# Kernel tuning notes

Hardware: AMD Instinct MI355X
Metric: run time of the kernel (lower is better)

The kernel has to match this reference:

```python
import jax, jax.numpy as jnp
import numpy as np

B, T, S = 128, 512, 30      # batch, input temporal length, sensor channels
F_NUM, KS, NL = 64, 5, 4    # conv filters, kernel size, n conv layers
H, NC = 128, 18             # GRU hidden dim, n classes


def setup_inputs() -> dict:
    key = jax.random.key(0)
    ks = jax.random.split(key, 16)
    r = lambda i, shape, s=0.05: (jax.random.normal(ks[i], shape, jnp.float32) * s)
    return {
        "x": jax.random.normal(ks[0], (B, 1, T, S), jnp.float32),
        "conv0_w": r(1, (F_NUM, 1, KS, 1), 0.2),          # first Conv2d (in=1)
        "convs_w": r(2, (3, F_NUM, F_NUM, KS, 1), 0.05),  # conv layers 1..3
        "conv_b": r(3, (NL, F_NUM)),
        "bn_gamma": jnp.ones((NL, F_NUM), jnp.float32),
        "bn_beta": jnp.zeros((NL, F_NUM), jnp.float32),
        "bn_mean": jnp.zeros((NL, F_NUM), jnp.float32),
        "bn_var": jnp.ones((NL, F_NUM), jnp.float32),
        "wq": r(4, (F_NUM, F_NUM), 0.1),
        "wk": r(5, (F_NUM, F_NUM), 0.1),
        "wv": r(6, (F_NUM, F_NUM), 0.1),
        "sa_gamma": jnp.array([0.1], jnp.float32),
        "fc1_w": r(7, (H, S * F_NUM), 0.02),
        "fc1_b": r(8, (H,)),
        "gru_wih": r(9, (2, 3 * H, H), 0.05),
        "gru_whh": r(10, (2, 3 * H, H), 0.05),
        "gru_bih": r(11, (2, 3 * H)),
        "gru_bhh": r(12, (2, 3 * H)),
        "pred_w": r(13, (NC, H), 0.05),
        "pred_b": r(14, (NC,)),
    }


def reference(x, conv0_w, convs_w, conv_b, bn_gamma, bn_beta, bn_mean, bn_var,
              wq, wk, wv, sa_gamma, fc1_w, fc1_b,
              gru_wih, gru_whh, gru_bih, gru_bhh, pred_w, pred_b):
    eps = 1e-5

    def conv_relu_bn(y, w, b, g, be, m, v):
        # Conv2d kernel (KS,1) stride (2,1), then ReLU, then BatchNorm (eval mode)
        y = jax.lax.conv_general_dilated(
            y, w, (2, 1), 'VALID',
            dimension_numbers=('NCHW', 'OIHW', 'NCHW')) + b[None, :, None, None]
        y = jax.nn.relu(y)
        inv = g / jnp.sqrt(v + eps)
        return y * inv[None, :, None, None] + (be - m * inv)[None, :, None, None]

    x = conv_relu_bn(x, conv0_w, conv_b[0], bn_gamma[0], bn_beta[0], bn_mean[0], bn_var[0])
    for i in range(3):  # fixed small layer loop
        x = conv_relu_bn(x, convs_w[i], conv_b[i + 1], bn_gamma[i + 1],
                         bn_beta[i + 1], bn_mean[i + 1], bn_var[i + 1])

    Bn, Fn, Ln, Sn = x.shape
    # Fold time into batch: per-timestep SelfAttention over (F, S) slices, vectorized
    xs = jnp.transpose(x, (0, 2, 1, 3)).reshape(Bn * Ln, Fn, Sn)  # (N, F, S)
    f = jnp.einsum('of,nfs->nos', wq, xs)   # query (1x1 conv1d, no bias)
    g = jnp.einsum('of,nfs->nos', wk, xs)   # key
    h = jnp.einsum('of,nfs->nos', wv, xs)   # value
    scores = jnp.einsum('noi,noj->nij', f, g)         # bmm(f^T, g): (N, S, S)
    beta = jax.nn.softmax(scores, axis=1)             # softmax over dim=1 (as torch)
    o = sa_gamma[0] * jnp.einsum('nfi,nij->nfj', h, beta) + xs  # (N, F, S)

    # cat over t then permute(0,3,1,2).reshape == (B, L, F*S)
    seq = o.reshape(Bn, Ln, Fn * Sn)
    seq = jax.nn.relu(seq @ fc1_w.T + fc1_b)          # (B, L, H); dropout = eval noop
    xs_t = jnp.transpose(seq, (1, 0, 2))              # (L, B, H) seq-first for GRU

    def gru_layer(xseq, wih, whh, bih, bhh):
        Hd = whh.shape[1]
        def step(hprev, xt):
            gi = xt @ wih.T + bih
            gh = hprev @ whh.T + bhh
            ir, iz, inn = jnp.split(gi, 3, axis=-1)
            hr, hz, hn = jnp.split(gh, 3, axis=-1)
            r = jax.nn.sigmoid(ir + hr)
            z = jax.nn.sigmoid(iz + hz)
            n = jnp.tanh(inn + r * hn)
            hnew = (1.0 - z) * n + z * hprev
            return hnew, hnew
        h0 = jnp.zeros((xseq.shape[1], Hd), xseq.dtype)
        _, ys = jax.lax.scan(step, h0, xseq)
        return ys

    for l in range(2):  # 2-layer GRU (inter-layer dropout = eval noop)
        xs_t = gru_layer(xs_t, gru_wih[l], gru_whh[l], gru_bih[l], gru_bhh[l])

    return xs_t[-1] @ pred_w.T + pred_b               # (B, NC)
```

## Files before the change

kernel.cpp:

```cpp
#include <hip/hip_runtime.h>
#include <math.h>

#define EPS 1e-5f

#define B_  128
#define T0_ 512
#define S_  30
#define F_  64
#define L1_ 254
#define L2_ 125
#define L3_ 61
#define L4_ 29
#define BS_ (B_*S_)
#define N_  (B_*L4_)
#define H_  128
#define NC_ 18
#define KFS 1920

typedef __attribute__((ext_vector_type(8))) short short8;
typedef __attribute__((ext_vector_type(16))) float f32x16;

__device__ __forceinline__ uint32_t f2bf(float f) {
    uint32_t u = __float_as_uint(f);
    return (u + 0x7fffu + ((u >> 16) & 1u)) >> 16;
}

typedef const __attribute__((address_space(1))) uint32_t* gas_t;
typedef __attribute__((address_space(3))) uint32_t* las_t;
__device__ __forceinline__ void glds16(const void* g, void* l) {
    __builtin_amdgcn_global_load_lds((gas_t)g, (las_t)l, 16, 0, 0);
}

#define MFMA(a,b,c) __builtin_amdgcn_mfma_f32_32x32x16_bf16(a, b, c, 0, 0, 0)

union ABu { uint4 u; short8 s; };

__global__ __launch_bounds__(256) void prepack_kernel(
    const float* __restrict__ wcs, ushort* __restrict__ aw)
{
    int i = blockIdx.x*256 + threadIdx.x;
    int l = i / 20480, r = i - l*20480;
    int j = r & 7, f = (r >> 3) & 63, g = r >> 9;
    int chalf = g & 1, ck = (g >> 1) & 3, kh = g >> 3;
    int c = ck*16 + chalf*8 + j;
    float w = wcs[l*20480 + f*320 + c*5 + kh];
    uint32_t h = f2bf(w);
    uint32_t lo = f2bf(w - __uint_as_float(h << 16));
    aw[l*40960 + r]         = (ushort)h;
    aw[l*40960 + 20480 + r] = (ushort)lo;
}

__device__ __forceinline__ void load_areg(const ushort* __restrict__ aw_l,
                                          int f0, int tcol, int chalf,
                                          ABu* AH_, ABu* AL_)
{
    #pragma unroll
    for (int idx = 0; idx < 20; idx++) {
        int r = (idx*2 + chalf)*512 + (f0 + tcol)*8;
        AH_[idx].u = *(const uint4*)(aw_l + r);
        AL_[idx].u = *(const uint4*)(aw_l + 20480 + r);
    }
}

__device__ __forceinline__ f32x16 conv_mm_reg(
    const ABu* AH_, const ABu* AL_,
    const ushort* __restrict__ Bh, const ushort* __restrict__ Bl,
    int t, int chalf)
{
    f32x16 acc;
    #pragma unroll
    for (int i = 0; i < 16; i++) acc[i] = 0.f;
    #pragma unroll
    for (int kh = 0; kh < 5; kh++) {
        int tp = 2*t + kh;
        int sw = (tp >> 3) & 7;
        const ushort* brh = Bh + tp*64;
        const ushort* brl = Bl + tp*64;
        #pragma unroll
        for (int ck = 0; ck < 4; ck++) {
            int idx = kh*4 + ck;
            int col = (((ck*2 + chalf) ^ sw) << 3);
            short8 BH = *(const short8*)(brh + col);
            short8 BL = *(const short8*)(brl + col);
            acc = MFMA(AH_[idx].s, BH, acc);
            acc = MFMA(AH_[idx].s, BL, acc);
            acc = MFMA(AL_[idx].s, BH, acc);
        }
    }
    return acc;
}

__global__ __launch_bounds__(512, 2) void conv01_mfma(
    const float* __restrict__ x,  const float* __restrict__ w0,
    const ushort* __restrict__ aw, const float* __restrict__ cb,
    const float* __restrict__ bg, const float* __restrict__ bb,
    const float* __restrict__ bm, const float* __restrict__ bv,
    char* __restrict__ y1h, char* __restrict__ y1l)
{
    __shared__ ushort Yt[2][264*64];
    __shared__ float xl[T0_];
    __shared__ float ep0[64], ep1[64], ep2[64];
    int tid = threadIdx.x;
    int lane = tid & 63, wv = tid >> 6;
    int tcol = lane & 31, chalf = lane >> 5;
    int f0 = (wv>>2)*32, t0 = (wv&3)*32, t = t0 + tcol;

    ABu AH_[20], AL_[20];
    load_areg(aw, f0, tcol, chalf, AH_, AL_);

    int cq = tid & 15, tpb = tid >> 4, c0 = cq*4;
    float w0r[20], inv0[4], add0[4], b0r[4];
    #pragma unroll
    for (int j = 0; j < 4; j++) {
        int c = c0 + j;
        #pragma unroll
        for (int u = 0; u < 5; u++) w0r[j*5+u] = w0[c*5+u];
        float iv = bg[c]*rsqrtf(bv[c]+EPS);
        inv0[j] = iv; add0[j] = bb[c]-bm[c]*iv; b0r[j] = cb[c];
    }
    if (tid < 64) {
        float iv = bg[64+tid]*rsqrtf(bv[64+tid]+EPS);
        ep0[tid] = iv; ep1[tid] = bb[64+tid]-bm[64+tid]*iv; ep2[tid] = cb[64+tid];
    }

    for (int sl = 0; sl < 5; sl++) {
        int bs = blockIdx.x*5 + sl, b = bs/S_, s = bs - b*S_;
        xl[tid] = x[(b*T0_ + tid)*S_ + s];
        __syncthreads();
        #pragma unroll
        for (int k = 0; k < 9; k++) {
            int tp = tpb + k*32;
            if (tp < 264) {
                float v4[4];
                if (tp < L1_) {
                    float2 xa = *(const float2*)&xl[2*tp];
                    float2 xb = *(const float2*)&xl[2*tp+2];
                    float2 xc = *(const float2*)&xl[2*tp+4];
                    #pragma unroll
                    for (int j = 0; j < 4; j++) {
                        float a = b0r[j] + w0r[j*5]*xa.x + w0r[j*5+1]*xa.y
                                + w0r[j*5+2]*xb.x + w0r[j*5+3]*xb.y + w0r[j*5+4]*xc.x;
                        v4[j] = fmaxf(a, 0.f)*inv0[j] + add0[j];
                    }
                } else { v4[0]=v4[1]=v4[2]=v4[3]=0.f; }
                uint32_t h0=f2bf(v4[0]), h1=f2bf(v4[1]), h2=f2bf(v4[2]), h3=f2bf(v4[3]);
                uint2 H; H.x = h0|(h1<<16); H.y = h2|(h3<<16);
                uint2 L;
                L.x = f2bf(v4[0]-__uint_as_float(h0<<16)) | (f2bf(v4[1]-__uint_as_float(h1<<16))<<16);
                L.y = f2bf(v4[2]-__uint_as_float(h2<<16)) | (f2bf(v4[3]-__uint_as_float(h3<<16))<<16);
                int pos = tp*64 + (c0 ^ (((tp>>3)&7)<<3));
                *(uint2*)&Yt[0][pos] = H;
                *(uint2*)&Yt[1][pos] = L;
            }
        }
        __syncthreads();
        f32x16 acc = conv_mm_reg(AH_, AL_, Yt[0], Yt[1], t, chalf);
        __syncthreads();
        if (t < L2_) {
            int swzo = ((t>>1) ^ (t>>3)) & 7;
            #pragma unroll
            for (int rq = 0; rq < 4; rq++) {
                int fb = f0 + 8*rq + 4*chalf;
                uint32_t h[4], l[4];
                #pragma unroll
                for (int j = 0; j < 4; j++) {
                    int r = rq*4 + j, f = fb + j;
                    float val = fmaxf(acc[r]+ep2[f], 0.f)*ep0[f] + ep1[f];
                    h[j] = f2bf(val);
                    l[j] = f2bf(val - __uint_as_float(h[j]<<16));
                }
                int pos = ((((fb>>3) ^ swzo) << 3) + (fb & 7));
                uint2 H; H.x = h[0] | (h[1]<<16); H.y = h[2] | (h[3]<<16);
                uint2 L; L.x = l[0] | (l[1]<<16); L.y = l[2] | (l[3]<<16);
                *(uint2*)&Yt[0][t*64 + pos] = H;
                *(uint2*)&Yt[1][t*64 + pos] = L;
            }
        }
        __syncthreads();
        for (int i = tid; i < 2000; i += 512) {
            int pl = i >= 1000, jj = pl ? i-1000 : i;
            int tr = jj >> 3, p = jj & 7;
            int q = p ^ ((tr>>1) & 7);
            uint4 v = *(const uint4*)&Yt[pl][tr*64 + q*8];
            *(uint4*)((pl ? y1l : y1h) + (size_t)bs*16000 + tr*128 + p*16) = v;
        }
    }
}

__global__ __launch_bounds__(512, 2) void conv2_mfma(
    const ushort* __restrict__ aw, const float* __restrict__ cb,
    const float* __restrict__ bg, const float* __restrict__ bb,
    const float* __restrict__ bm, const float* __restrict__ bv,
    char* __restrict__ yh, char* __restrict__ yl)
{
    __shared__ ushort Yt[2][2][2][132*64];
    __shared__ float ep0[64], ep1[64], ep2[64];
    int tid = threadIdx.x;
    int lane = tid & 63, wv = tid >> 6;
    int tcol = lane & 31, chalf = lane >> 5;
    int slw = wv >> 2, f0 = ((wv>>1)&1)*32, t0 = (wv&1)*32, t = t0 + tcol;
    int blk = blockIdx.x;

    ABu AH_[20], AL_[20];
    load_areg(aw + 40960, f0, tcol, chalf, AH_, AL_);
    if (tid < 64) {
        float iv = bg[128+tid]*rsqrtf(bv[128+tid]+EPS);
        ep0[tid] = iv; ep1[tid] = bb[128+tid]-bm[128+tid]*iv; ep2[tid] = cb[128+tid];
    }
    #pragma unroll
    for (int sl2 = 0; sl2 < 2; sl2++)
        #pragma unroll
        for (int pl = 0; pl < 2; pl++) {
            const char* src = (pl ? yl : yh) + (size_t)(blk*8 + sl2)*16000;
            glds16(src + tid*16,        (char*)&Yt[0][sl2][pl][0] + (tid>>6)*1024);
            glds16(src + 8192 + tid*16, (char*)&Yt[0][sl2][pl][0] + 8192 + (tid>>6)*1024);
        }
    for (int i = tid; i < 1024; i += 512) {
        int g = i >> 7, w2 = i & 127;
        ((uint32_t*)&Yt[g>>2][(g>>1)&1][g&1][128*64])[w2] = 0;
    }
    __syncthreads();
    for (int i = tid; i < 384; i += 512) {
        int g = i / 96, w2 = i - g*96;
        ((uint32_t*)&Yt[0][g>>1][g&1][125*64])[w2] = 0;
    }
    __syncthreads();

    for (int it = 0; it < 4; it++) {
        int buf = it & 1;
        int bs0 = blk*8 + it*2;
        if (it < 3) {
            #pragma unroll
            for (int sl2 = 0; sl2 < 2; sl2++)
                #pragma unroll
                for (int pl = 0; pl < 2; pl++) {
                    const char* src = (pl ? yl : yh) + (size_t)(bs0 + 2 + sl2)*16000;
                    glds16(src + tid*16,        (char*)&Yt[buf^1][sl2][pl][0] + (tid>>6)*1024);
                    glds16(src + 8192 + tid*16, (char*)&Yt[buf^1][sl2][pl][0] + 8192 + (tid>>6)*1024);
                }
        }
        f32x16 acc = conv_mm_reg(AH_, AL_, Yt[buf][slw][0], Yt[buf][slw][1], t, chalf);
        __syncthreads();
        if (it < 3) {
            for (int i = tid; i < 384; i += 512) {
                int g = i / 96, w2 = i - g*96;
                ((uint32_t*)&Yt[buf^1][g>>1][g&1][125*64])[w2] = 0;
            }
        }
        if (t < L3_) {
            int swzo = ((t>>1) ^ (t>>3)) & 7;
            #pragma unroll
            for (int rq = 0; rq < 4; rq++) {
                int fb = f0 + 8*rq + 4*chalf;
                uint32_t h[4], l[4];
                #pragma unroll
                for (int j = 0; j < 4; j++) {
                    int r = rq*4 + j, f = fb + j;
                    float val = fmaxf(acc[r]+ep2[f], 0.f)*ep0[f] + ep1[f];
                    h[j] = f2bf(val);
                    l[j] = f2bf(val - __uint_as_float(h[j]<<16));
                }
                int pos = ((((fb>>3) ^ swzo) << 3) + (fb & 7));
                uint2 H; H.x = h[0] | (h[1]<<16); H.y = h[2] | (h[3]<<16);
                uint2 L; L.x = l[0] | (l[1]<<16); L.y = l[2] | (l[3]<<16);
                *(uint2*)&Yt[buf][slw][0][t*64 + pos] = H;
                *(uint2*)&Yt[buf][slw][1][t*64 + pos] = L;
            }
        }
        __syncthreads();
        for (int i = tid; i < 1952; i += 512) {
            int s2 = i / 976, r2 = i - s2*976;
            int pl = r2 >= 488, jj = pl ? r2-488 : r2;
            int tr = jj >> 3, p = jj & 7;
            int q = p ^ ((tr>>1) & 7);
            uint4 v = *(const uint4*)&Yt[buf][s2][pl][tr*64 + q*8];
            *(uint4*)((pl ? yl : yh) + (size_t)(bs0+s2)*16000 + tr*128 + p*16) = v;
        }
        __syncthreads();
    }
}

__global__ __launch_bounds__(512, 2) void conv3_mfma(
    const ushort* __restrict__ aw, const float* __restrict__ cb,
    const float* __restrict__ bg, const float* __restrict__ bb,
    const float* __restrict__ bm, const float* __restrict__ bv,
    const char* __restrict__ yh, const char* __restrict__ yl,
    float* __restrict__ y3)
{
    __shared__ ushort Yt[2][4][2][68*64];
    __shared__ float ep0[64], ep1[64], ep2[64];
    int tid = threadIdx.x;
    int lane = tid & 63, wv = tid >> 6;
    int tcol = lane & 31, chalf = lane >> 5;
    int slq = wv >> 1, f0 = (wv&1)*32, t = tcol;
    int blk = blockIdx.x;

    ABu AH_[20], AL_[20];
    load_areg(aw + 81920, f0, tcol, chalf, AH_, AL_);
    if (tid < 64) {
        float iv = bg[192+tid]*rsqrtf(bv[192+tid]+EPS);
        ep0[tid] = iv; ep1[tid] = bb[192+tid]-bm[192+tid]*iv; ep2[tid] = cb[192+tid];
    }
    #pragma unroll
    for (int sl2 = 0; sl2 < 4; sl2++)
        #pragma unroll
        for (int pl = 0; pl < 2; pl++) {
            const char* src = (pl ? yl : yh) + (size_t)(blk*8 + sl2)*16000;
            glds16(src + tid*16, (char*)&Yt[0][sl2][pl][0] + (tid>>6)*1024);
        }
    for (int i = tid; i < 2048; i += 512) {
        int g = i >> 7, w2 = i & 127;
        ((uint32_t*)&Yt[g>>3][(g>>1)&3][g&1][64*64])[w2] = 0;
    }
    __syncthreads();
    for (int i = tid; i < 768; i += 512) {
        int g = i / 96, w2 = i - g*96;
        ((uint32_t*)&Yt[0][g>>1][g&1][61*64])[w2] = 0;
    }
    __syncthreads();

    for (int it = 0; it < 2; it++) {
        int buf = it & 1;
        int bs0 = blk*8 + it*4;
        if (it < 1) {
            #pragma unroll
            for (int sl2 = 0; sl2 < 4; sl2++)
                #pragma unroll
                for (int pl = 0; pl < 2; pl++) {
                    const char* src = (pl ? yl : yh) + (size_t)(bs0 + 4 + sl2)*16000;
                    glds16(src + tid*16, (char*)&Yt[buf^1][sl2][pl][0] + (tid>>6)*1024);
                }
        }
        f32x16 acc = conv_mm_reg(AH_, AL_, Yt[buf][slq][0], Yt[buf][slq][1], t, chalf);
        if (t < L4_) {
            #pragma unroll
            for (int r = 0; r < 16; r++) {
                int f = f0 + (r&3) + 8*(r>>2) + 4*chalf;
                float val = fmaxf(acc[r]+ep2[f], 0.f)*ep0[f] + ep1[f];
                y3[((size_t)(bs0+slq)*F_ + f)*L4_ + t] = val;
            }
        }
        __syncthreads();
        if (it < 1) {
            for (int i = tid; i < 768; i += 512) {
                int g = i / 96, w2 = i - g*96;
                ((uint32_t*)&Yt[buf^1][g>>1][g&1][61*64])[w2] = 0;
            }
        }
        __syncthreads();
    }
}

__global__ __launch_bounds__(256) void transp_kernel(
    const float* __restrict__ y3, float* __restrict__ xs)
{
    __shared__ float tl[15*F_*L4_];
    int b = blockIdx.x >> 1, s0 = (blockIdx.x & 1)*15;
    int tid = threadIdx.x;
    const float* src = y3 + (b*S_ + s0)*F_*L4_;
    for (int i = tid; i < 15*F_*L4_; i += 256) tl[i] = src[i];
    __syncthreads();
    for (int i = tid; i < L4_*F_*15; i += 256) {
        int l = i/(F_*15), f = (i/15)%F_, ss = i%15;
        xs[((b*L4_+l)*F_+f)*S_ + s0+ss] = tl[(ss*F_+f)*L4_ + l];
    }
}

__global__ __launch_bounds__(256) void attn_kernel(
    const float* __restrict__ xsg, const float* __restrict__ wq,
    const float* __restrict__ wk,  const float* __restrict__ wv,
    const float* __restrict__ gam, float* __restrict__ seq)
{
    __shared__ float X[F_][32];
    __shared__ float QKV[192][36];
    __shared__ float BETA[S_][36];
    int n = blockIdx.x, tid = threadIdx.x;
    for (int i = tid; i < KFS; i += 256) X[i/S_][i%S_] = xsg[n*KFS + i];
    for (int i = tid; i < 128; i += 256) X[i>>1][30 + (i&1)] = 0.f;
    __syncthreads();
    if (tid < 192) {
        int wsel = tid >> 6, row = tid & 63;
        const float* W = (wsel==0) ? wq : (wsel==1) ? wk : wv;
        float4 wr_[16];
        #pragma unroll
        for (int u = 0; u < 16; u++) wr_[u] = ((const float4*)(W + row*64))[u];
        float acc[32];
        #pragma unroll
        for (int i = 0; i < 32; i++) acc[i] = 0.f;
        #pragma unroll
        for (int u = 0; u < 16; u++) {
            float4 w4 = wr_[u];
            #pragma unroll
            for (int c = 0; c < 4; c++) {
                float wv_ = (c==0) ? w4.x : (c==1) ? w4.y : (c==2) ? w4.z : w4.w;
                const float4* xr = (const float4*)&X[u*4+c][0];
                #pragma unroll
                for (int q = 0; q < 8; q++) {
                    float4 xq = xr[q];
                    acc[q*4+0] += wv_*xq.x; acc[q*4+1] += wv_*xq.y;
                    acc[q*4+2] += wv_*xq.z; acc[q*4+3] += wv_*xq.w;
                }
            }
        }
        #pragma unroll
        for (int q = 0; q < 8; q++) {
            float4 o4; o4.x=acc[q*4]; o4.y=acc[q*4+1]; o4.z=acc[q*4+2]; o4.w=acc[q*4+3];
            *(float4*)&QKV[tid][q*4] = o4;
        }
    }
    __syncthreads();
    if (tid < 240) {
        int j = tid >> 3, iq = tid & 7;
        float4 s4 = {0.f, 0.f, 0.f, 0.f};
        for (int o = 0; o < 64; o++) {
            float4 q4 = *(const float4*)&QKV[o][iq*4];
            float kv = QKV[64+o][j];
            s4.x += q4.x*kv; s4.y += q4.y*kv; s4.z += q4.z*kv; s4.w += q4.w*kv;
        }
        if (iq == 7) { s4.z = -1e30f; s4.w = -1e30f; }
        float m = fmaxf(fmaxf(s4.x, s4.y), fmaxf(s4.z, s4.w));
        m = fmaxf(m, __shfl_xor(m, 1, 8));
        m = fmaxf(m, __shfl_xor(m, 2, 8));
        m = fmaxf(m, __shfl_xor(m, 4, 8));
        float e0 = expf(s4.x-m), e1 = expf(s4.y-m), e2 = expf(s4.z-m), e3 = expf(s4.w-m);
        if (iq == 7) { e2 = 0.f; e3 = 0.f; }
        float sum = e0+e1+e2+e3;
        sum += __shfl_xor(sum, 1, 8);
        sum += __shfl_xor(sum, 2, 8);
        sum += __shfl_xor(sum, 4, 8);
        float inv = 1.f/sum;
        int i0 = iq*4;
        BETA[i0][j]   = e0*inv;
        BETA[i0+1][j] = e1*inv;
        if (iq < 7) { BETA[i0+2][j] = e2*inv; BETA[i0+3][j] = e3*inv; }
    }
    __syncthreads();
    {
        int f = tid >> 2, jh = tid & 3;
        float acc[8];
        #pragma unroll
        for (int i = 0; i < 8; i++) acc[i] = 0.f;
        for (int i = 0; i < S_; i++) {
            float v = QKV[128+f][i];
            float4 b0 = *(const float4*)&BETA[i][jh*8];
            float4 b1 = *(const float4*)&BETA[i][jh*8+4];
            acc[0] += v*b0.x; acc[1] += v*b0.y; acc[2] += v*b0.z; acc[3] += v*b0.w;
            acc[4] += v*b1.x; acc[5] += v*b1.y; acc[6] += v*b1.z; acc[7] += v*b1.w;
        }
        float g = gam[0];
        int j0 = jh*8;
        #pragma unroll
        for (int jj = 0; jj < 8; jj++) {
            int j = j0 + jj;
            if (j < S_) seq[n*KFS + f*S_ + j] = g*acc[jj] + X[f][j];
        }
    }
}

__global__ __launch_bounds__(256) void fc1_kernel(
    const float* __restrict__ seq, const float* __restrict__ w,
    const float* __restrict__ bias, float* __restrict__ out)
{
    __shared__ float Sm[8*KFS];
    int n0 = blockIdx.x*8, tid = threadIdx.x;
    for (int i = tid; i < 8*KFS; i += 256) Sm[i] = seq[n0*KFS + i];
    __syncthreads();
    int h = tid & 127, rp = tid >> 7;
    float acc[4] = {0,0,0,0};
    const float4* wp = (const float4*)(w + h*KFS);
    #pragma unroll 4
    for (int k = 0; k < KFS/4; k++) {
        float4 wvv = wp[k];
        #pragma unroll
        for (int j = 0; j < 4; j++) {
            float4 sv = ((const float4*)&Sm[(rp*4+j)*KFS])[k];
            acc[j] += wvv.x*sv.x + wvv.y*sv.y + wvv.z*sv.z + wvv.w*sv.w;
        }
    }
    float bb2 = bias[h];
    #pragma unroll
    for (int j = 0; j < 4; j++)
        out[(n0 + rp*4 + j)*H_ + h] = fmaxf(acc[j] + bb2, 0.f);
}

__global__ __launch_bounds__(768) void gru_kernel(
    const float* __restrict__ xin,  const float* __restrict__ wih,
    const float* __restrict__ whh,  const float* __restrict__ bih,
    const float* __restrict__ bhh,  const float* __restrict__ pw,
    const float* __restrict__ pb,   float* __restrict__ out)
{
    __shared__ float xh[H_], hh[H_], gi[3*H_], gh[3*H_], ys[L4_][H_];
    int b = blockIdx.x, tid = threadIdx.x;
    int mat = tid / 384, j = tid % 384;
    float4 wr[32];
    for (int layer = 0; layer < 2; layer++) {
        const float* wsrc = (mat ? whh : wih) + layer*384*128 + j*128;
        #pragma unroll
        for (int u = 0; u < 32; u++) wr[u] = ((const float4*)wsrc)[u];
        float bias = (mat ? bhh : bih)[layer*384 + j];
        if (tid < H_) hh[tid] = 0.f;
        __syncthreads();
        for (int t = 0; t < L4_; t++) {
            if (tid < H_) xh[tid] = (layer == 0) ? xin[(b*L4_+t)*H_ + tid] : ys[t][tid];
            __syncthreads();
            const float* src = mat ? hh : xh;
            float a0=0,a1=0,a2=0,a3=0;
            #pragma unroll
            for (int u = 0; u < 32; u++) {
                float4 xv = ((const float4*)src)[u];
                a0 += wr[u].x*xv.x; a1 += wr[u].y*xv.y;
                a2 += wr[u].z*xv.z; a3 += wr[u].w*xv.w;
            }
            float g = (a0+a1)+(a2+a3) + bias;
            if (mat) gh[j] = g; else gi[j] = g;
            __syncthreads();
            if (tid < H_) {
                int m = tid;
                float r = 1.f/(1.f+expf(-(gi[m]      + gh[m])));
                float z = 1.f/(1.f+expf(-(gi[m+128]  + gh[m+128])));
                float n = tanhf(gi[m+256] + r*gh[m+256]);
                float hnew = (1.f-z)*n + z*hh[m];
                hh[m] = hnew; ys[t][m] = hnew;
            }
            __syncthreads();
        }
    }
    if (tid < NC_) {
        float a = pb[tid];
        for (int k = 0; k < H_; k++) a += pw[tid*H_+k]*hh[k];
        out[b*NC_ + tid] = a;
    }
}

extern "C" void kernel_launch(void* const* d_in, const int* in_sizes, int n_in,
                              void* d_out, int out_size, void* d_ws, size_t ws_size,
                              hipStream_t stream) {
    const float* x    = (const float*)d_in[0];
    const float* w0   = (const float*)d_in[1];
    const float* wcs  = (const float*)d_in[2];
    const float* cb   = (const float*)d_in[3];
    const float* bg   = (const float*)d_in[4];
    const float* bb   = (const float*)d_in[5];
    const float* bm   = (const float*)d_in[6];
    const float* bv   = (const float*)d_in[7];
    const float* wq   = (const float*)d_in[8];
    const float* wk   = (const float*)d_in[9];
    const float* wv   = (const float*)d_in[10];
    const float* gam  = (const float*)d_in[11];
    const float* fw   = (const float*)d_in[12];
    const float* fb   = (const float*)d_in[13];
    const float* gwih = (const float*)d_in[14];
    const float* gwhh = (const float*)d_in[15];
    const float* gbih = (const float*)d_in[16];
    const float* gbhh = (const float*)d_in[17];
    const float* pw   = (const float*)d_in[18];
    const float* pb   = (const float*)d_in[19];
    float* out = (float*)d_out;
    uint32_t* wsu = (uint32_t*)d_ws;

    ushort* aw  = (ushort*)wsu;
    char* y1h   = (char*)(wsu + 61440);
    char* y1l   = (char*)(wsu + 15425536);
    float* y3v  = (float*)(wsu + 30789632);
    float* seqv = (float*)(wsu + 30789632);
    float* xsv  = (float*)(wsu + 37916672);
    float* f1v  = (float*)(wsu + 37916672);

    prepack_kernel<<<240, 256, 0, stream>>>(wcs, aw);
    conv01_mfma<<<768, 512, 0, stream>>>(x, w0, aw, cb, bg, bb, bm, bv, y1h, y1l);
    conv2_mfma<<<480, 512, 0, stream>>>(aw, cb, bg, bb, bm, bv, y1h, y1l);
    conv3_mfma<<<480, 512, 0, stream>>>(aw, cb, bg, bb, bm, bv, y1h, y1l, y3v);
    transp_kernel<<<2*B_, 256, 0, stream>>>(y3v, xsv);
    attn_kernel<<<N_, 256, 0, stream>>>(xsv, wq, wk, wv, gam, seqv);
    fc1_kernel<<<N_/8, 256, 0, stream>>>(seqv, fw, fb, f1v);
    gru_kernel<<<B_, 768, 0, stream>>>(f1v, gwih, gwhh, gbih, gbhh, pw, pb, out);
}
```

Before: 726.7 us.

## Restructure conv MFMA kernels to 256-thread blocks with swizzled intermediate layout

The conv0/1, conv2 and conv3 MFMA kernels move from 512-thread blocks to 256-thread blocks. Each wave now computes more time columns (conv01 runs two MFMA passes per wave), and conv2 processes one slice per iteration with double buffering. Intermediate activations are stored in a padded, already-swizzled 16384-byte-per-slice layout, so the copy-out no longer unswizzles and loads can use aligned 4 KiB chunks. Float-to-bf16 hi/lo splitting now truncates via byte permutes instead of rounding, and workspace offsets are reshuffled. The aim is to raise occupancy and cut epilogue ALU and LDS traffic, at the cost of fewer waves per block, more serial MFMA work per wave, and slightly different rounding of the split.

```diff
diff --git a/kernel.cpp b/kernel.cpp
--- a/kernel.cpp
+++ b/kernel.cpp
@@ -90,7 +90,34 @@
     return acc;
 }
 
-__global__ __launch_bounds__(512, 2) void conv01_mfma(
+__device__ __forceinline__ void epi_pack_store(const f32x16& acc, int t, int f0, int chalf,
+    const float* __restrict__ e0, const float* __restrict__ e1, const float* __restrict__ e2,
+    ushort* __restrict__ Y0, ushort* __restrict__ Y1)
+{
+    int sw = (t >> 3) & 7;
+    #pragma unroll
+    for (int rq = 0; rq < 4; rq++) {
+        int fb = f0 + 8*rq + 4*chalf;
+        uint32_t u[4], r[4];
+        #pragma unroll
+        for (int j = 0; j < 4; j++) {
+            int f = fb + j;
+            float v = fmaxf(acc[rq*4+j] + e2[f], 0.f)*e0[f] + e1[f];
+            u[j] = __float_as_uint(v);
+            r[j] = __float_as_uint(v - __uint_as_float(u[j] & 0xffff0000u));
+        }
+        uint2 H, L;
+        H.x = __builtin_amdgcn_perm(u[1], u[0], 0x07060302u);
+        H.y = __builtin_amdgcn_perm(u[3], u[2], 0x07060302u);
+        L.x = __builtin_amdgcn_perm(r[1], r[0], 0x07060302u);
+        L.y = __builtin_amdgcn_perm(r[3], r[2], 0x07060302u);
+        int pos = t*64 + (((fb >> 3) ^ sw) << 3) + (fb & 7);
+        *(uint2*)&Y0[pos] = H;
+        *(uint2*)&Y1[pos] = L;
+    }
+}
+
+__global__ __launch_bounds__(256) void conv01_mfma(
     const float* __restrict__ x,  const float* __restrict__ w0,
     const ushort* __restrict__ aw, const float* __restrict__ cb,
     const float* __restrict__ bg, const float* __restrict__ bb,
@@ -103,126 +130,172 @@
     int tid = threadIdx.x;
     int lane = tid & 63, wv = tid >> 6;
     int tcol = lane & 31, chalf = lane >> 5;
-    int f0 = (wv>>2)*32, t0 = (wv&3)*32, t = t0 + tcol;
+    int f0 = (wv & 1)*32;
+    int tA = (wv >> 1)*32 + tcol;
+    int tB = tA + 64;
 
     ABu AH_[20], AL_[20];
     load_areg(aw, f0, tcol, chalf, AH_, AL_);
 
-    int cq = tid & 15, tpb = tid >> 4, c0 = cq*4;
-    float w0r[20], inv0[4], add0[4], b0r[4];
-    #pragma unroll
-    for (int j = 0; j < 4; j++) {
-        int c = c0 + j;
-        #pragma unroll
-        for (int u = 0; u < 5; u++) w0r[j*5+u] = w0[c*5+u];
-        float iv = bg[c]*rsqrtf(bv[c]+EPS);
-        inv0[j] = iv; add0[j] = bb[c]-bm[c]*iv; b0r[j] = cb[c];
+    int c2 = (tid & 31)*2, tq = tid >> 5;
+    float w0p[10], bi[2], iv[2], ad[2];
+    #pragma unroll
+    for (int j = 0; j < 2; j++) {
+        int c = c2 + j;
+        #pragma unroll
+        for (int u = 0; u < 5; u++) w0p[j*5+u] = w0[c*5+u];
+        float v = bg[c]*rsqrtf(bv[c]+EPS);
+        iv[j] = v; ad[j] = bb[c]-bm[c]*v; bi[j] = cb[c];
     }
     if (tid < 64) {
-        float iv = bg[64+tid]*rsqrtf(bv[64+tid]+EPS);
-        ep0[tid] = iv; ep1[tid] = bb[64+tid]-bm[64+tid]*iv; ep2[tid] = cb[64+tid];
+        float v = bg[64+tid]*rsqrtf(bv[64+tid]+EPS);
+        ep0[tid] = v; ep1[tid] = bb[64+tid]-bm[64+tid]*v; ep2[tid] = cb[64+tid];
     }
 
     for (int sl = 0; sl < 5; sl++) {
         int bs = blockIdx.x*5 + sl, b = bs/S_, s = bs - b*S_;
-        xl[tid] = x[(b*T0_ + tid)*S_ + s];
-        __syncthreads();
-        #pragma unroll
-        for (int k = 0; k < 9; k++) {
-            int tp = tpb + k*32;
-            if (tp < 264) {
-                float v4[4];
-                if (tp < L1_) {
-                    float2 xa = *(const float2*)&xl[2*tp];
-                    float2 xb = *(const float2*)&xl[2*tp+2];
-                    float2 xc = *(const float2*)&xl[2*tp+4];
-                    #pragma unroll
-                    for (int j = 0; j < 4; j++) {
-                        float a = b0r[j] + w0r[j*5]*xa.x + w0r[j*5+1]*xa.y
-                                + w0r[j*5+2]*xb.x + w0r[j*5+3]*xb.y + w0r[j*5+4]*xc.x;
-                        v4[j] = fmaxf(a, 0.f)*inv0[j] + add0[j];
-                    }
-                } else { v4[0]=v4[1]=v4[2]=v4[3]=0.f; }
-                uint32_t h0=f2bf(v4[0]), h1=f2bf(v4[1]), h2=f2bf(v4[2]), h3=f2bf(v4[3]);
-                uint2 H; H.x = h0|(h1<<16); H.y = h2|(h3<<16);
-                uint2 L;
-                L.x = f2bf(v4[0]-__uint_as_float(h0<<16)) | (f2bf(v4[1]-__uint_as_float(h1<<16))<<16);
-                L.y = f2bf(v4[2]-__uint_as_float(h2<<16)) | (f2bf(v4[3]-__uint_as_float(h3<<16))<<16);
-                int pos = tp*64 + (c0 ^ (((tp>>3)&7)<<3));
-                *(uint2*)&Yt[0][pos] = H;
-                *(uint2*)&Yt[1][pos] = L;
-            }
-        }
-        __syncthreads();
-        f32x16 acc = conv_mm_reg(AH_, AL_, Yt[0], Yt[1], t, chalf);
-        __syncthreads();
-        if (t < L2_) {
-            int swzo = ((t>>1) ^ (t>>3)) & 7;
-            #pragma unroll
-            for (int rq = 0; rq < 4; rq++) {
-                int fb = f0 + 8*rq + 4*chalf;
-                uint32_t h[4], l[4];
-                #pragma unroll
-                for (int j = 0; j < 4; j++) {
-                    int r = rq*4 + j, f = fb + j;
-                    float val = fmaxf(acc[r]+ep2[f], 0.f)*ep0[f] + ep1[f];
-                    h[j] = f2bf(val);
-                    l[j] = f2bf(val - __uint_as_float(h[j]<<16));
-                }
-                int pos = ((((fb>>3) ^ swzo) << 3) + (fb & 7));
-                uint2 H; H.x = h[0] | (h[1]<<16); H.y = h[2] | (h[3]<<16);
-                uint2 L; L.x = l[0] | (l[1]<<16); L.y = l[2] | (l[3]<<16);
-                *(uint2*)&Yt[0][t*64 + pos] = H;
-                *(uint2*)&Yt[1][t*64 + pos] = L;
-            }
-        }
-        __syncthreads();
-        for (int i = tid; i < 2000; i += 512) {
-            int pl = i >= 1000, jj = pl ? i-1000 : i;
+        xl[tid]       = x[(b*T0_ + tid)*S_ + s];
+        xl[tid + 256] = x[(b*T0_ + tid + 256)*S_ + s];
+        __syncthreads();
+        for (int k = 0; k < 33; k++) {
+            int tp = tq + k*8;
+            uint32_t Hw = 0, Lw = 0;
+            if (tp < L1_) {
+                float2 xa = *(const float2*)&xl[2*tp];
+                float2 xb = *(const float2*)&xl[2*tp+2];
+                float xc = xl[2*tp+4];
+                float v0 = bi[0] + w0p[0]*xa.x + w0p[1]*xa.y + w0p[2]*xb.x + w0p[3]*xb.y + w0p[4]*xc;
+                float v1 = bi[1] + w0p[5]*xa.x + w0p[6]*xa.y + w0p[7]*xb.x + w0p[8]*xb.y + w0p[9]*xc;
+                v0 = fmaxf(v0, 0.f)*iv[0] + ad[0];
+                v1 = fmaxf(v1, 0.f)*iv[1] + ad[1];
+                uint32_t u0 = __float_as_uint(v0), u1 = __float_as_uint(v1);
+                Hw = __builtin_amdgcn_perm(u1, u0, 0x07060302u);
+                uint32_t r0 = __float_as_uint(v0 - __uint_as_float(u0 & 0xffff0000u));
+                uint32_t r1 = __float_as_uint(v1 - __uint_as_float(u1 & 0xffff0000u));
+                Lw = __builtin_amdgcn_perm(r1, r0, 0x07060302u);
+            }
+            int pos = tp*64 + (c2 ^ (((tp>>3)&7) << 3));
+            *(uint32_t*)&Yt[0][pos] = Hw;
+            *(uint32_t*)&Yt[1][pos] = Lw;
+        }
+        __syncthreads();
+        f32x16 acc0 = conv_mm_reg(AH_, AL_, Yt[0], Yt[1], tA, chalf);
+        __syncthreads();
+        epi_pack_store(acc0, tA, f0, chalf, ep0, ep1, ep2, Yt[0], Yt[1]);
+        f32x16 acc1 = conv_mm_reg(AH_, AL_, Yt[0], Yt[1], tB, chalf);
+        if (tB < L2_) epi_pack_store(acc1, tB, f0, chalf, ep0, ep1, ep2, Yt[0], Yt[1]);
+        __syncthreads();
+        for (int i = tid; i < 2048; i += 256) {
+            int pl = i >> 10, jj = i & 1023;
             int tr = jj >> 3, p = jj & 7;
-            int q = p ^ ((tr>>1) & 7);
-            uint4 v = *(const uint4*)&Yt[pl][tr*64 + q*8];
-            *(uint4*)((pl ? y1l : y1h) + (size_t)bs*16000 + tr*128 + p*16) = v;
-        }
-    }
-}
-
-__global__ __launch_bounds__(512, 2) void conv2_mfma(
+            uint4 v = *(const uint4*)&Yt[pl][tr*64 + p*8];
+            *(uint4*)((pl ? y1l : y1h) + (size_t)bs*16384 + tr*128 + p*16) = v;
+        }
+        __syncthreads();
+    }
+}
+
+__global__ __launch_bounds__(256) void conv2_mfma(
     const ushort* __restrict__ aw, const float* __restrict__ cb,
     const float* __restrict__ bg, const float* __restrict__ bb,
     const float* __restrict__ bm, const float* __restrict__ bv,
     char* __restrict__ yh, char* __restrict__ yl)
 {
-    __shared__ ushort Yt[2][2][2][132*64];
+    __shared__ ushort Yt[2][2][132*64];
     __shared__ float ep0[64], ep1[64], ep2[64];
     int tid = threadIdx.x;
     int lane = tid & 63, wv = tid >> 6;
     int tcol = lane & 31, chalf = lane >> 5;
-    int slw = wv >> 2, f0 = ((wv>>1)&1)*32, t0 = (wv&1)*32, t = t0 + tcol;
+    int f0 = (wv & 1)*32;
+    int t = (wv >> 1)*32 + tcol;
     int blk = blockIdx.x;
 
     ABu AH_[20], AL_[20];
     load_areg(aw + 40960, f0, tcol, chalf, AH_, AL_);
     if (tid < 64) {
-        float iv = bg[128+tid]*rsqrtf(bv[128+tid]+EPS);
-        ep0[tid] = iv; ep1[tid] = bb[128+tid]-bm[128+tid]*iv; ep2[tid] = cb[128+tid];
-    }
-    #pragma unroll
-    for (int sl2 = 0; sl2 < 2; sl2++)
+        float v = bg[128+tid]*rsqrtf(bv[128+tid]+EPS);
+        ep0[tid] = v; ep1[tid] = bb[128+tid]-bm[128+tid]*v; ep2[tid] = cb[128+tid];
+    }
+    #pragma unroll
+    for (int pl = 0; pl < 2; pl++) {
+        const char* src = (pl ? yl : yh) + (size_t)(blk*8)*16384;
+        #pragma unroll
+        for (int k = 0; k < 4; k++)
+            glds16(src + k*4096 + tid*16, (char*)&Yt[0][pl][0] + k*4096 + (tid>>6)*1024);
+    }
+    __syncthreads();
+    for (int i = tid; i < 448; i += 256) {
+        int pl = i >= 224, jj = pl ? i-224 : i;
+        ((uint32_t*)&Yt[0][pl][125*64])[jj] = 0;
+    }
+    __syncthreads();
+
+    for (int it = 0; it < 8; it++) {
+        int buf = it & 1;
+        int bs = blk*8 + it;
+        if (it < 7) {
+            #pragma unroll
+            for (int pl = 0; pl < 2; pl++) {
+                const char* src = (pl ? yl : yh) + (size_t)(bs+1)*16384;
+                #pragma unroll
+                for (int k = 0; k < 4; k++)
+                    glds16(src + k*4096 + tid*16, (char*)&Yt[buf^1][pl][0] + k*4096 + (tid>>6)*1024);
+            }
+        }
+        f32x16 acc = conv_mm_reg(AH_, AL_, Yt[buf][0], Yt[buf][1], t, chalf);
+        __syncthreads();
+        if (it < 7) {
+            for (int i = tid; i < 448; i += 256) {
+                int pl = i >= 224, jj = pl ? i-224 : i;
+                ((uint32_t*)&Yt[buf^1][pl][125*64])[jj] = 0;
+            }
+        }
+        if (t < L3_) epi_pack_store(acc, t, f0, chalf, ep0, ep1, ep2, Yt[buf][0], Yt[buf][1]);
+        __syncthreads();
+        for (int i = tid; i < 976; i += 256) {
+            int pl = i >= 488, jj = pl ? i-488 : i;
+            int tr = jj >> 3, p = jj & 7;
+            uint4 v = *(const uint4*)&Yt[buf][pl][tr*64 + p*8];
+            *(uint4*)((pl ? yl : yh) + (size_t)bs*16384 + tr*128 + p*16) = v;
+        }
+        __syncthreads();
+    }
+}
+
+__global__ __launch_bounds__(256) void conv3_mfma(
+    const ushort* __restrict__ aw, const float* __restrict__ cb,
+    const float* __restrict__ bg, const float* __restrict__ bb,
+    const float* __restrict__ bm, const float* __restrict__ bv,
+    const char* __restrict__ yh, const char* __restrict__ yl,
+    float* __restrict__ y3)
+{
+    __shared__ ushort Yt[2][2][2][68*64];
+    __shared__ float ep0[64], ep1[64], ep2[64];
+    int tid = threadIdx.x;
+    int lane = tid & 63, wv = tid >> 6;
+    int tcol = lane & 31, chalf = lane >> 5;
+    int f0 = (wv & 1)*32, slw = wv >> 1, t = tcol;
+    int blk = blockIdx.x;
+
+    ABu AH_[20], AL_[20];
+    load_areg(aw + 81920, f0, tcol, chalf, AH_, AL_);
+    if (tid < 64) {
+        float v = bg[192+tid]*rsqrtf(bv[192+tid]+EPS);
+        ep0[tid] = v; ep1[tid] = bb[192+tid]-bm[192+tid]*v; ep2[tid] = cb[192+tid];
+    }
+    #pragma unroll
+    for (int sl = 0; sl < 2; sl++)
         #pragma unroll
         for (int pl = 0; pl < 2; pl++) {
-            const char* src = (pl ? yl : yh) + (size_t)(blk*8 + sl2)*16000;
-            glds16(src + tid*16,        (char*)&Yt[0][sl2][pl][0] + (tid>>6)*1024);
-            glds16(src + 8192 + tid*16, (char*)&Yt[0][sl2][pl][0] + 8192 + (tid>>6)*1024);
-        }
-    for (int i = tid; i < 1024; i += 512) {
-        int g = i >> 7, w2 = i & 127;
-        ((uint32_t*)&Yt[g>>2][(g>>1)&1][g&1][128*64])[w2] = 0;
-    }
-    __syncthreads();
-    for (int i = tid; i < 384; i += 512) {
-        int g = i / 96, w2 = i - g*96;
-        ((uint32_t*)&Yt[0][g>>1][g&1][125*64])[w2] = 0;
+            const char* src = (pl ? yl : yh) + (size_t)(blk*8 + sl)*16384;
+            #pragma unroll
+            for (int k = 0; k < 2; k++)
+                glds16(src + k*4096 + tid*16, (char*)&Yt[0][sl][pl][0] + k*4096 + (tid>>6)*1024);
+        }
+    __syncthreads();
+    for (int i = tid; i < 896; i += 256) {
+        int g = i / 224, jj = i - g*224;
+        ((uint32_t*)&Yt[0][g>>1][g&1][61*64])[jj] = 0;
     }
     __syncthreads();
 
@@ -231,120 +304,29 @@
         int bs0 = blk*8 + it*2;
         if (it < 3) {
             #pragma unroll
-            for (int sl2 = 0; sl2 < 2; sl2++)
+            for (int sl = 0; sl < 2; sl++)
                 #pragma unroll
                 for (int pl = 0; pl < 2; pl++) {
-                    const char* src = (pl ? yl : yh) + (size_t)(bs0 + 2 + sl2)*16000;
-                    glds16(src + tid*16,        (char*)&Yt[buf^1][sl2][pl][0] + (tid>>6)*1024);
-                    glds16(src + 8192 + tid*16, (char*)&Yt[buf^1][sl2][pl][0] + 8192 + (tid>>6)*1024);
+                    const char* src = (pl ? yl : yh) + (size_t)(bs0 + 2 + sl)*16384;
+                    #pragma unroll
+                    for (int k = 0; k < 2; k++)
+                        glds16(src + k*4096 + tid*16, (char*)&Yt[buf^1][sl][pl][0] + k*4096 + (tid>>6)*1024);
                 }
         }
         f32x16 acc = conv_mm_reg(AH_, AL_, Yt[buf][slw][0], Yt[buf][slw][1], t, chalf);
-        __syncthreads();
-        if (it < 3) {
-            for (int i = tid; i < 384; i += 512) {
-                int g = i / 96, w2 = i - g*96;
-                ((uint32_t*)&Yt[buf^1][g>>1][g&1][125*64])[w2] = 0;
-            }
-        }
-        if (t < L3_) {
-            int swzo = ((t>>1) ^ (t>>3)) & 7;
-            #pragma unroll
-            for (int rq = 0; rq < 4; rq++) {
-                int fb = f0 + 8*rq + 4*chalf;
-                uint32_t h[4], l[4];
-                #pragma unroll
-                for (int j = 0; j < 4; j++) {
-                    int r = rq*4 + j, f = fb + j;
-                    float val = fmaxf(acc[r]+ep2[f], 0.f)*ep0[f] + ep1[f];
-                    h[j] = f2bf(val);
-                    l[j] = f2bf(val - __uint_as_float(h[j]<<16));
-                }
-                int pos = ((((fb>>3) ^ swzo) << 3) + (fb & 7));
-                uint2 H; H.x = h[0] | (h[1]<<16); H.y = h[2] | (h[3]<<16);
-                uint2 L; L.x = l[0] | (l[1]<<16); L.y = l[2] | (l[3]<<16);
-                *(uint2*)&Yt[buf][slw][0][t*64 + pos] = H;
-                *(uint2*)&Yt[buf][slw][1][t*64 + pos] = L;
-            }
-        }
-        __syncthreads();
-        for (int i = tid; i < 1952; i += 512) {
-            int s2 = i / 976, r2 = i - s2*976;
-            int pl = r2 >= 488, jj = pl ? r2-488 : r2;
-            int tr = jj >> 3, p = jj & 7;
-            int q = p ^ ((tr>>1) & 7);
-            uint4 v = *(const uint4*)&Yt[buf][s2][pl][tr*64 + q*8];
-            *(uint4*)((pl ? yl : yh) + (size_t)(bs0+s2)*16000 + tr*128 + p*16) = v;
-        }
-        __syncthreads();
-    }
-}
-
-__global__ __launch_bounds__(512, 2) void conv3_mfma(
-    const ushort* __restrict__ aw, const float* __restrict__ cb,
-    const float* __restrict__ bg, const float* __restrict__ bb,
-    const float* __restrict__ bm, const float* __restrict__ bv,
-    const char* __restrict__ yh, const char* __restrict__ yl,
-    float* __restrict__ y3)
-{
-    __shared__ ushort Yt[2][4][2][68*64];
-    __shared__ float ep0[64], ep1[64], ep2[64];
-    int tid = threadIdx.x;
-    int lane = tid & 63, wv = tid >> 6;
-    int tcol = lane & 31, chalf = lane >> 5;
-    int slq = wv >> 1, f0 = (wv&1)*32, t = tcol;
-    int blk = blockIdx.x;
-
-    ABu AH_[20], AL_[20];
-    load_areg(aw + 81920, f0, tcol, chalf, AH_, AL_);
-    if (tid < 64) {
-        float iv = bg[192+tid]*rsqrtf(bv[192+tid]+EPS);
-        ep0[tid] = iv; ep1[tid] = bb[192+tid]-bm[192+tid]*iv; ep2[tid] = cb[192+tid];
-    }
-    #pragma unroll
-    for (int sl2 = 0; sl2 < 4; sl2++)
-        #pragma unroll
-        for (int pl = 0; pl < 2; pl++) {
-            const char* src = (pl ? yl : yh) + (size_t)(blk*8 + sl2)*16000;
-            glds16(src + tid*16, (char*)&Yt[0][sl2][pl][0] + (tid>>6)*1024);
-        }
-    for (int i = tid; i < 2048; i += 512) {
-        int g = i >> 7, w2 = i & 127;
-        ((uint32_t*)&Yt[g>>3][(g>>1)&3][g&1][64*64])[w2] = 0;
-    }
-    __syncthreads();
-    for (int i = tid; i < 768; i += 512) {
-        int g = i / 96, w2 = i - g*96;
-        ((uint32_t*)&Yt[0][g>>1][g&1][61*64])[w2] = 0;
-    }
-    __syncthreads();
-
-    for (int it = 0; it < 2; it++) {
-        int buf = it & 1;
-        int bs0 = blk*8 + it*4;
-        if (it < 1) {
-            #pragma unroll
-            for (int sl2 = 0; sl2 < 4; sl2++)
-                #pragma unroll
-                for (int pl = 0; pl < 2; pl++) {
-                    const char* src = (pl ? yl : yh) + (size_t)(bs0 + 4 + sl2)*16000;
-                    glds16(src + tid*16, (char*)&Yt[buf^1][sl2][pl][0] + (tid>>6)*1024);
-                }
-        }
-        f32x16 acc = conv_mm_reg(AH_, AL_, Yt[buf][slq][0], Yt[buf][slq][1], t, chalf);
         if (t < L4_) {
             #pragma unroll
             for (int r = 0; r < 16; r++) {
                 int f = f0 + (r&3) + 8*(r>>2) + 4*chalf;
                 float val = fmaxf(acc[r]+ep2[f], 0.f)*ep0[f] + ep1[f];
-                y3[((size_t)(bs0+slq)*F_ + f)*L4_ + t] = val;
-            }
-        }
-        __syncthreads();
-        if (it < 1) {
-            for (int i = tid; i < 768; i += 512) {
-                int g = i / 96, w2 = i - g*96;
-                ((uint32_t*)&Yt[buf^1][g>>1][g&1][61*64])[w2] = 0;
+                y3[((size_t)(bs0+slw)*F_ + f)*L4_ + t] = val;
+            }
+        }
+        __syncthreads();
+        if (it < 3) {
+            for (int i = tid; i < 896; i += 256) {
+                int g = i / 224, jj = i - g*224;
+                ((uint32_t*)&Yt[buf^1][g>>1][g&1][61*64])[jj] = 0;
             }
         }
         __syncthreads();
@@ -560,16 +542,16 @@
 
     ushort* aw  = (ushort*)wsu;
     char* y1h   = (char*)(wsu + 61440);
-    char* y1l   = (char*)(wsu + 15425536);
-    float* y3v  = (float*)(wsu + 30789632);
-    float* seqv = (float*)(wsu + 30789632);
-    float* xsv  = (float*)(wsu + 37916672);
-    float* f1v  = (float*)(wsu + 37916672);
+    char* y1l   = (char*)(wsu + 15790080);
+    float* y3v  = (float*)(wsu + 31518720);
+    float* xsv  = (float*)(wsu + 61440);
+    float* seqv = (float*)(wsu + 7188480);
+    float* f1v  = (float*)(wsu + 14315520);
 
     prepack_kernel<<<240, 256, 0, stream>>>(wcs, aw);
-    conv01_mfma<<<768, 512, 0, stream>>>(x, w0, aw, cb, bg, bb, bm, bv, y1h, y1l);
-    conv2_mfma<<<480, 512, 0, stream>>>(aw, cb, bg, bb, bm, bv, y1h, y1l);
-    conv3_mfma<<<480, 512, 0, stream>>>(aw, cb, bg, bb, bm, bv, y1h, y1l, y3v);
+    conv01_mfma<<<768, 256, 0, stream>>>(x, w0, aw, cb, bg, bb, bm, bv, y1h, y1l);
+    conv2_mfma<<<480, 256, 0, stream>>>(aw, cb, bg, bb, bm, bv, y1h, y1l);
+    conv3_mfma<<<480, 256, 0, stream>>>(aw, cb, bg, bb, bm, bv, y1h, y1l, y3v);
     transp_kernel<<<2*B_, 256, 0, stream>>>(y3v, xsv);
     attn_kernel<<<N_, 256, 0, stream>>>(xsv, wq, wk, wv, gam, seqv);
     fc1_kernel<<<N_/8, 256, 0, stream>>>(seqv, fw, fb, f1v);
```

Result: faster. 678.3 us (-6.7%).
